# Performance work log

Measured on AMD Instinct MI355X. Metric: run time of the kernel, lower is better.

Reference implementation:

```python
import jax, jax.numpy as jnp
import numpy as np

NUM_HEADS = 16
EMBED = 1024
HEAD = EMBED // NUM_HEADS


def setup_inputs() -> dict:
    key = jax.random.key(0)
    ks = jax.random.split(key, 9)
    s = 1.0 / np.sqrt(EMBED)
    inp = {
        "x": jax.random.normal(ks[0], (2, 2048, EMBED), dtype=jnp.float32),
        "Wq": jax.random.normal(ks[1], (EMBED, EMBED), dtype=jnp.float32) * s,
        "bq": jax.random.normal(ks[2], (EMBED,), dtype=jnp.float32) * s,
        "Wk": jax.random.normal(ks[3], (EMBED, EMBED), dtype=jnp.float32) * s,
        "bk": jax.random.normal(ks[4], (EMBED,), dtype=jnp.float32) * s,
        "Wv": jax.random.normal(ks[5], (EMBED, EMBED), dtype=jnp.float32) * s,
        "bv": jax.random.normal(ks[6], (EMBED,), dtype=jnp.float32) * s,
        "Wo": jax.random.normal(ks[7], (EMBED, EMBED), dtype=jnp.float32) * s,
        "bo": jax.random.normal(ks[8], (EMBED,), dtype=jnp.float32) * s,
    }
    return inp


def reference(x, Wq, bq, Wk, bk, Wv, bv, Wo, bo):
    B, S, E = x.shape
    H, D = NUM_HEADS, HEAD
    # QKV projections ([in,out] layout -> x @ W + b)
    Q = (x @ Wq + bq).reshape(B, S, H, D).transpose(0, 2, 1, 3)  # [B,H,S,D]
    K = (x @ Wk + bk).reshape(B, S, H, D).transpose(0, 2, 1, 3)
    V = (x @ Wv + bv).reshape(B, S, H, D).transpose(0, 2, 1, 3)
    scores = jnp.einsum("bhqd,bhkd->bhqk", Q, K) / jnp.sqrt(jnp.float32(D))
    # causal mask: positions k > q are masked (strict upper triangle)
    causal = jnp.tril(jnp.ones((S, S), dtype=bool))
    scores = jnp.where(causal, scores, jnp.float32(-jnp.inf))
    attn = jax.nn.softmax(scores, axis=-1)
    out = jnp.einsum("bhqk,bhkd->bhqd", attn, V)
    out = out.transpose(0, 2, 1, 3).reshape(B, S, E)
    return out @ Wo + bo
```

## Files before the change

kernel.cpp:

```cpp
#include <hip/hip_runtime.h>


using f32x4  = __attribute__((ext_vector_type(4))) float;
using bf16x8 = __attribute__((ext_vector_type(8))) __bf16;
using u16x8  = __attribute__((ext_vector_type(8))) unsigned short;
using u32x4  = __attribute__((ext_vector_type(4))) unsigned int;

__device__ __forceinline__ unsigned short f2bf(float f) {
  unsigned u = __float_as_uint(f);
  u += 0x7fff + ((u >> 16) & 1u);
  return (unsigned short)(u >> 16);
}

__device__ __forceinline__ unsigned short bfc(float f) {
  __bf16 h = (__bf16)f;
  return __builtin_bit_cast(unsigned short, h);
}

__device__ __forceinline__ bf16x8 ld_bf8(const unsigned short* p) {
  return __builtin_bit_cast(bf16x8, *reinterpret_cast<const u16x8*>(p));
}

#define GLDS16(gp, lp)                                                        \
  __builtin_amdgcn_global_load_lds(                                           \
      (__attribute__((address_space(1))) void*)(gp),                          \
      (__attribute__((address_space(3))) void*)(lp), 16, 0, 0)

__global__ void cast_x_kernel(const float* __restrict__ src,
                              unsigned short* __restrict__ dst) {
  const int i = (blockIdx.x * 256 + threadIdx.x) * 4;
  const float4 v = *reinterpret_cast<const float4*>(src + i);
  ushort4 o;
  o.x = f2bf(v.x); o.y = f2bf(v.y); o.z = f2bf(v.z); o.w = f2bf(v.w);
  *reinterpret_cast<ushort4*>(dst + i) = o;
}

__global__ void cast_wt_kernel(const float* __restrict__ w0, const float* __restrict__ w1,
                               const float* __restrict__ w2, const float* __restrict__ w3,
                               unsigned short* __restrict__ t0, unsigned short* __restrict__ t1,
                               unsigned short* __restrict__ t2, unsigned short* __restrict__ t3) {
  const float* src; unsigned short* dst;
  switch (blockIdx.z) {
    case 0:  src = w0; dst = t0; break;
    case 1:  src = w1; dst = t1; break;
    case 2:  src = w2; dst = t2; break;
    default: src = w3; dst = t3; break;
  }
  __shared__ float tile[64][65];
  const int n0 = blockIdx.x * 64, k0 = blockIdx.y * 64;
  const int t = threadIdx.x;
#pragma unroll
  for (int i = 0; i < 4; ++i) {
    const int q = t + i * 256, r = q >> 4, c4 = q & 15;
    const float4 v = *reinterpret_cast<const float4*>(src + (k0 + r) * 1024 + n0 + c4 * 4);
    tile[r][c4 * 4 + 0] = v.x; tile[r][c4 * 4 + 1] = v.y;
    tile[r][c4 * 4 + 2] = v.z; tile[r][c4 * 4 + 3] = v.w;
  }
  __syncthreads();
#pragma unroll
  for (int i = 0; i < 4; ++i) {
    const int q = t + i * 256, n = q >> 4, c4 = q & 15;
    ushort4 o;
    o.x = f2bf(tile[c4 * 4 + 0][n]); o.y = f2bf(tile[c4 * 4 + 1][n]);
    o.z = f2bf(tile[c4 * 4 + 2][n]); o.w = f2bf(tile[c4 * 4 + 3][n]);
    *reinterpret_cast<ushort4*>(dst + (n0 + n) * 1024 + k0 + c4 * 4) = o;
  }
}

template <int MODE>
__global__ __launch_bounds__(256, 2) void gemm128(
    const unsigned short* __restrict__ A,
    const unsigned short* __restrict__ BtQ, const unsigned short* __restrict__ BtK,
    const unsigned short* __restrict__ BtV,
    const float* __restrict__ biasQ, const float* __restrict__ biasK,
    const float* __restrict__ biasV,
    unsigned short* __restrict__ OQ, unsigned short* __restrict__ OK_,
    unsigned short* __restrict__ OV, float* __restrict__ OF) {
  __shared__ unsigned short As[128 * 64];
  __shared__ unsigned short Bs[128 * 64];

  const int mt = blockIdx.x, nt = blockIdx.y;
  const unsigned short* Bt; const float* bias;
  unsigned short* Obf = nullptr;
  int nloc0;
  float scl = 1.0f;
  if (MODE == 0) {
    const int which = nt >> 3;
    nloc0 = (nt & 7) * 128;
    Bt   = (which == 0) ? BtQ   : (which == 1) ? BtK   : BtV;
    bias = (which == 0) ? biasQ : (which == 1) ? biasK : biasV;
    Obf  = (which == 0) ? OQ    : (which == 1) ? OK_   : OV;
    if (which == 0) scl = 0.18033688f;
  } else {
    nloc0 = nt * 128;
    Bt = BtQ; bias = biasQ;
  }
  const int m0 = mt * 128;
  const int t = threadIdx.x;
  const int w = t >> 6, l = t & 63;
  const int wm = (w >> 1) * 64, wn = (w & 1) * 64;
  const int lr = l & 15, lg = l >> 4;

  f32x4 acc[4][4];
#pragma unroll
  for (int i = 0; i < 4; ++i)
#pragma unroll
    for (int j = 0; j < 4; ++j) acc[i][j] = f32x4{0.f, 0.f, 0.f, 0.f};

  for (int k0 = 0; k0 < 1024; k0 += 64) {
#pragma unroll
    for (int i = 0; i < 4; ++i) {
      const int off = t * 16 + i * 4096;
      const int r = off >> 7, cb = off & 127;
      GLDS16(A + (m0 + r) * 1024 + k0 + (cb >> 1), ((char*)As) + off);
    }
#pragma unroll
    for (int i = 0; i < 4; ++i) {
      const int off = t * 16 + i * 4096;
      const int r = off >> 7, cb = off & 127;
      GLDS16(Bt + (nloc0 + r) * 1024 + k0 + (cb >> 1), ((char*)Bs) + off);
    }
    __syncthreads();
#pragma unroll
    for (int kk = 0; kk < 2; ++kk) {
      bf16x8 af[4], bfr[4];
#pragma unroll
      for (int mi = 0; mi < 4; ++mi)
        af[mi] = ld_bf8(As + (wm + mi * 16 + lr) * 64 + kk * 32 + lg * 8);
#pragma unroll
      for (int ni = 0; ni < 4; ++ni)
        bfr[ni] = ld_bf8(Bs + (wn + ni * 16 + lr) * 64 + kk * 32 + lg * 8);
#pragma unroll
      for (int mi = 0; mi < 4; ++mi)
#pragma unroll
        for (int ni = 0; ni < 4; ++ni)
          acc[mi][ni] = __builtin_amdgcn_mfma_f32_16x16x32_bf16(af[mi], bfr[ni], acc[mi][ni], 0, 0, 0);
    }
    __syncthreads();
  }

#pragma unroll
  for (int ni = 0; ni < 4; ++ni) {
    const int n = nloc0 + wn + ni * 16 + lr;
    const float bv = bias[n];
#pragma unroll
    for (int mi = 0; mi < 4; ++mi) {
#pragma unroll
      for (int r = 0; r < 4; ++r) {
        const int m = m0 + wm + mi * 16 + 4 * lg + r;
        const float v = (acc[mi][ni][r] + bv) * scl;
        if (MODE == 0) {
          const int b = m >> 11, s = m & 2047;
          const int h = n >> 6,  d = n & 63;
          Obf[(((b * 16 + h) * 2048) + s) * 64 + d] = f2bf(v);
        } else {
          OF[m * 1024 + n] = v;
        }
      }
    }
  }
}

__global__ void transpose_v_kernel(const unsigned short* __restrict__ Vh,
                                   unsigned short* __restrict__ Vt) {
  const int bh = blockIdx.y;
  const int s0 = blockIdx.x * 64;
  __shared__ unsigned short tile[64][72];
  const int t = threadIdx.x;
#pragma unroll
  for (int i = 0; i < 4; ++i) {
    const int q = t + i * 256, r = q >> 4, c4 = q & 15;
    const ushort4 v = *reinterpret_cast<const ushort4*>(Vh + ((size_t)bh * 2048 + s0 + r) * 64 + c4 * 4);
    tile[r][c4 * 4 + 0] = v.x; tile[r][c4 * 4 + 1] = v.y;
    tile[r][c4 * 4 + 2] = v.z; tile[r][c4 * 4 + 3] = v.w;
  }
  __syncthreads();
#pragma unroll
  for (int i = 0; i < 4; ++i) {
    const int q = t + i * 256, d = q >> 4, c4 = q & 15;
    ushort4 o;
    o.x = tile[c4 * 4 + 0][d]; o.y = tile[c4 * 4 + 1][d];
    o.z = tile[c4 * 4 + 2][d]; o.w = tile[c4 * 4 + 3][d];
    *reinterpret_cast<ushort4*>(Vt + ((size_t)bh * 64 + d) * 2048 + s0 + c4 * 4) = o;
  }
}

__global__ __launch_bounds__(256, 4) void attn_kernel(
    const unsigned short* __restrict__ Qh, const unsigned short* __restrict__ Kh,
    const unsigned short* __restrict__ Vt, unsigned short* __restrict__ Ob) {
  const int g = blockIdx.x;
  const int qt = 31 - (g >> 5);
  const int bh = g & 31;
  const int b = bh >> 4, h = bh & 15;
  const int t = threadIdx.x, w = t >> 6, l = t & 63;
  const int lr = l & 15, lg = l >> 4;
  const int sl0 = lr + 32 * (lg & 1);
  const int sl1 = sl0 + 16;
  const bool hi2 = (l & 32) != 0;

  __shared__ unsigned short Kb[2][4096];
  __shared__ unsigned short Vb[2][4096];

  const unsigned short* Kbase = Kh + (size_t)bh * (2048 * 64);
  const unsigned short* Vbase = Vt + (size_t)bh * (64 * 2048);

  const int qb = qt * 64 + w * 16;
  const unsigned short* Qp = Qh + ((size_t)bh * 2048 + qb + lr) * 64;
  bf16x8 qf[2];
  qf[0] = ld_bf8(Qp + lg * 8);
  qf[1] = ld_bf8(Qp + 32 + lg * 8);

  f32x4 oacc[4];
#pragma unroll
  for (int i = 0; i < 4; ++i) oacc[i] = f32x4{0.f, 0.f, 0.f, 0.f};
  float mrun = -3e38f;
  float lpart = 0.f;

  auto stage = [&](int kv0, int bi) {
#pragma unroll
    for (int p = 0; p < 2; ++p) {
      const int o = t * 16 + p * 4096;
      const int row = o >> 7;
      const int scb = (o & 127) ^ ((row & 7) << 4);
      GLDS16(Kbase + (size_t)(kv0 + row) * 64 + (scb >> 1), ((char*)Kb[bi]) + o);
      GLDS16(Vbase + (size_t)row * 2048 + kv0 + (scb >> 1), ((char*)Vb[bi]) + o);
    }
  };

  const int nt = qt + 1;
  stage(0, 0);
  __syncthreads();

  for (int ti = 0; ti < nt; ++ti) {
    const int cur = ti & 1;
    const int kv0 = ti * 64;
    if (ti + 1 < nt) stage((ti + 1) * 64, cur ^ 1);

    f32x4 s[4];
#pragma unroll
    for (int i = 0; i < 4; ++i) s[i] = f32x4{0.f, 0.f, 0.f, 0.f};
    __builtin_amdgcn_s_setprio(1);
#pragma unroll
    for (int kf = 0; kf < 2; ++kf) {
#pragma unroll
      for (int nf = 0; nf < 4; ++nf) {
        const int row = nf * 16 + lr;
        const int col = (kf * 32 + lg * 8) ^ ((row & 7) << 3);
        const bf16x8 kb = ld_bf8(&Kb[cur][row * 64 + col]);
        s[nf] = __builtin_amdgcn_mfma_f32_16x16x32_bf16(kb, qf[kf], s[nf], 0, 0, 0);
      }
    }
    __builtin_amdgcn_s_setprio(0);

    if (ti == qt) {
#pragma unroll
      for (int nf = 0; nf < 4; ++nf) {
        const int kv = kv0 + nf * 16 + 4 * lg;
#pragma unroll
        for (int r = 0; r < 4; ++r)
          if (kv + r > qb + lr) s[nf][r] = -3e38f;
      }
    }
    float m01 = -3e38f, m23 = -3e38f;
#pragma unroll
    for (int r = 0; r < 4; ++r) {
      m01 = fmaxf(m01, fmaxf(s[0][r], s[1][r]));
      m23 = fmaxf(m23, fmaxf(s[2][r], s[3][r]));
    }
    const float mx = fmaxf(m01, m23);
    if (!__all(mx <= mrun + 8.f)) {
      float m0 = fmaxf(mx, __shfl_xor(mx, 16));
      m0 = fmaxf(m0, __shfl_xor(m0, 32));
      const float n0 = fmaxf(mrun, m0);
      const float c0 = __builtin_amdgcn_exp2f(mrun - n0);
      mrun = n0;
      lpart *= c0;
#pragma unroll
      for (int df = 0; df < 4; ++df)
#pragma unroll
        for (int r = 0; r < 4; ++r) oacc[df][r] *= c0;
    }
    float rs[4] = {0.f, 0.f, 0.f, 0.f};
#pragma unroll
    for (int nf = 0; nf < 4; ++nf)
#pragma unroll
      for (int r = 0; r < 4; ++r) {
        const float p = __builtin_amdgcn_exp2f(s[nf][r] - mrun);
        s[nf][r] = p;
        rs[nf] += p;
      }
    lpart += (rs[0] + rs[1]) + (rs[2] + rs[3]);

    unsigned wpk[4][2];
#pragma unroll
    for (int nf = 0; nf < 4; ++nf) {
      asm("v_cvt_pk_bf16_f32 %0, %1, %2" : "=v"(wpk[nf][0]) : "v"(s[nf][0]), "v"(s[nf][1]));
      asm("v_cvt_pk_bf16_f32 %0, %1, %2" : "=v"(wpk[nf][1]) : "v"(s[nf][2]), "v"(s[nf][3]));
    }
    bf16x8 pa[2];
#pragma unroll
    for (int kf = 0; kf < 2; ++kf) {
      const unsigned a0w = __shfl(wpk[2 * kf][0], sl0), b0w = __shfl(wpk[2 * kf + 1][0], sl0);
      const unsigned a1w = __shfl(wpk[2 * kf][1], sl0), b1w = __shfl(wpk[2 * kf + 1][1], sl0);
      const unsigned a2w = __shfl(wpk[2 * kf][0], sl1), b2w = __shfl(wpk[2 * kf + 1][0], sl1);
      const unsigned a3w = __shfl(wpk[2 * kf][1], sl1), b3w = __shfl(wpk[2 * kf + 1][1], sl1);
      u32x4 uu;
      uu[0] = hi2 ? b0w : a0w;
      uu[1] = hi2 ? b1w : a1w;
      uu[2] = hi2 ? b2w : a2w;
      uu[3] = hi2 ? b3w : a3w;
      pa[kf] = __builtin_bit_cast(bf16x8, uu);
    }

    __builtin_amdgcn_s_setprio(1);
#pragma unroll
    for (int kf = 0; kf < 2; ++kf) {
#pragma unroll
      for (int df = 0; df < 4; ++df) {
        const int vrow = df * 16 + lr;
        const int vcol = (kf * 32 + lg * 8) ^ ((vrow & 7) << 3);
        const bf16x8 vb = ld_bf8(&Vb[cur][vrow * 64 + vcol]);
        oacc[df] = __builtin_amdgcn_mfma_f32_16x16x32_bf16(vb, pa[kf], oacc[df], 0, 0, 0);
      }
    }
    __builtin_amdgcn_s_setprio(0);
    __syncthreads();
  }

  float ls = lpart;
  ls += __shfl_xor(ls, 16);
  ls += __shfl_xor(ls, 32);
  const float inv = 1.f / ls;
  const int q = qb + lr;
#pragma unroll
  for (int df = 0; df < 4; ++df) {
    ushort4 o4;
    o4.x = bfc(oacc[df][0] * inv);
    o4.y = bfc(oacc[df][1] * inv);
    o4.z = bfc(oacc[df][2] * inv);
    o4.w = bfc(oacc[df][3] * inv);
    *reinterpret_cast<ushort4*>(
        &Ob[((size_t)(b * 2048 + q)) * 1024 + h * 64 + df * 16 + 4 * lg]) = o4;
  }
}

extern "C" void kernel_launch(void* const* d_in, const int* in_sizes, int n_in,
                              void* d_out, int out_size, void* d_ws, size_t ws_size,
                              hipStream_t stream) {
  const float* x  = (const float*)d_in[0];
  const float* Wq = (const float*)d_in[1];
  const float* bq = (const float*)d_in[2];
  const float* Wk = (const float*)d_in[3];
  const float* bk = (const float*)d_in[4];
  const float* Wv = (const float*)d_in[5];
  const float* bv = (const float*)d_in[6];
  const float* Wo = (const float*)d_in[7];
  const float* bo = (const float*)d_in[8];
  float* out = (float*)d_out;

  unsigned short* xb  = (unsigned short*)d_ws;
  unsigned short* wqt = xb  + 4096 * 1024;
  unsigned short* wkt = wqt + 1024 * 1024;
  unsigned short* wvt = wkt + 1024 * 1024;
  unsigned short* wot = wvt + 1024 * 1024;
  unsigned short* Qh  = wot + 1024 * 1024;
  unsigned short* Kh  = Qh  + 4096 * 1024;
  unsigned short* Vh  = Kh  + 4096 * 1024;
  unsigned short* Vt  = Vh  + 4096 * 1024;
  unsigned short* Ob  = Vt  + 4096 * 1024;

  cast_x_kernel<<<4096, 256, 0, stream>>>(x, xb);
  cast_wt_kernel<<<dim3(16, 16, 4), 256, 0, stream>>>(Wq, Wk, Wv, Wo, wqt, wkt, wvt, wot);
  gemm128<0><<<dim3(32, 24), 256, 0, stream>>>(xb, wqt, wkt, wvt, bq, bk, bv,
                                               Qh, Kh, Vh, nullptr);
  transpose_v_kernel<<<dim3(32, 32), 256, 0, stream>>>(Vh, Vt);
  attn_kernel<<<1024, 256, 0, stream>>>(Qh, Kh, Vt, Ob);
  gemm128<1><<<dim3(32, 8), 256, 0, stream>>>(Ob, wot, nullptr, nullptr, bo, nullptr, nullptr,
                                              nullptr, nullptr, nullptr, out);
}
```

Before: 121.2 us.

## Merge cast kernels, write V transposed from QKV GEMM, use 256-tile pipelined GEMM

Combines the x cast and weight transpose-casts into one launch. Replaces the 128x128 QKV GEMM with a 256x256 tile, 512-thread kernel that uses a 4-stage global-to-LDS pipeline, XOR-swizzled LDS, setprio around the MFMA blocks and a block-index remap. The V projection is now written straight into the transposed layout, so the separate transpose kernel and its extra pass over V are gone. The output projection becomes its own specialized kernel with occupancy raised to 3. The larger tiles cut global traffic and launch count, but the QKV GEMM now runs only 192 blocks at 1 block per CU, which may leave CUs underused.

```diff
diff --git a/kernel.cpp b/kernel.cpp
--- a/kernel.cpp
+++ b/kernel.cpp
@@ -26,29 +26,33 @@
       (__attribute__((address_space(1))) void*)(gp),                          \
       (__attribute__((address_space(3))) void*)(lp), 16, 0, 0)
 
-__global__ void cast_x_kernel(const float* __restrict__ src,
-                              unsigned short* __restrict__ dst) {
-  const int i = (blockIdx.x * 256 + threadIdx.x) * 4;
-  const float4 v = *reinterpret_cast<const float4*>(src + i);
-  ushort4 o;
-  o.x = f2bf(v.x); o.y = f2bf(v.y); o.z = f2bf(v.z); o.w = f2bf(v.w);
-  *reinterpret_cast<ushort4*>(dst + i) = o;
-}
-
-__global__ void cast_wt_kernel(const float* __restrict__ w0, const float* __restrict__ w1,
-                               const float* __restrict__ w2, const float* __restrict__ w3,
-                               unsigned short* __restrict__ t0, unsigned short* __restrict__ t1,
-                               unsigned short* __restrict__ t2, unsigned short* __restrict__ t3) {
+__global__ void prep_kernel(const float* __restrict__ x,
+                            const float* __restrict__ w0, const float* __restrict__ w1,
+                            const float* __restrict__ w2, const float* __restrict__ w3,
+                            unsigned short* __restrict__ xb,
+                            unsigned short* __restrict__ t0, unsigned short* __restrict__ t1,
+                            unsigned short* __restrict__ t2, unsigned short* __restrict__ t3) {
+  __shared__ float tile[64][65];
+  const int t = threadIdx.x;
+  const int bid = blockIdx.x;
+  if (bid < 4096) {
+    const int i = (bid * 256 + t) * 4;
+    const float4 v = *reinterpret_cast<const float4*>(x + i);
+    ushort4 o;
+    o.x = f2bf(v.x); o.y = f2bf(v.y); o.z = f2bf(v.z); o.w = f2bf(v.w);
+    *reinterpret_cast<ushort4*>(xb + i) = o;
+    return;
+  }
+  const int q0 = bid - 4096;
+  const int wsel = q0 >> 8, rem = q0 & 255;
   const float* src; unsigned short* dst;
-  switch (blockIdx.z) {
+  switch (wsel) {
     case 0:  src = w0; dst = t0; break;
     case 1:  src = w1; dst = t1; break;
     case 2:  src = w2; dst = t2; break;
     default: src = w3; dst = t3; break;
   }
-  __shared__ float tile[64][65];
-  const int n0 = blockIdx.x * 64, k0 = blockIdx.y * 64;
-  const int t = threadIdx.x;
+  const int n0 = (rem & 15) * 64, k0 = (rem >> 4) * 64;
 #pragma unroll
   for (int i = 0; i < 4; ++i) {
     const int q = t + i * 256, r = q >> 4, c4 = q & 15;
@@ -67,35 +71,152 @@
   }
 }
 
-template <int MODE>
-__global__ __launch_bounds__(256, 2) void gemm128(
+__global__ __launch_bounds__(512, 1) void gemm256_qkv(
     const unsigned short* __restrict__ A,
     const unsigned short* __restrict__ BtQ, const unsigned short* __restrict__ BtK,
     const unsigned short* __restrict__ BtV,
     const float* __restrict__ biasQ, const float* __restrict__ biasK,
     const float* __restrict__ biasV,
     unsigned short* __restrict__ OQ, unsigned short* __restrict__ OK_,
-    unsigned short* __restrict__ OV, float* __restrict__ OF) {
+    unsigned short* __restrict__ OVt) {
+  __shared__ unsigned short As[4][256 * 32];
+  __shared__ unsigned short Bs[4][256 * 32];
+
+  const int bid0 = blockIdx.x;
+  const int bid = (bid0 & 7) * 24 + (bid0 >> 3);
+  const int ntile = bid >> 4;
+  const int mtile = bid & 15;
+  const int which = ntile >> 2;
+  const unsigned short* Bt = (which == 0) ? BtQ : (which == 1) ? BtK : BtV;
+  const float* bias = (which == 0) ? biasQ : (which == 1) ? biasK : biasV;
+  const int nn = (ntile & 3) * 256;
+  const int m0 = mtile * 256;
+
+  const int tid = threadIdx.x;
+  const int w = tid >> 6, l = tid & 63;
+  const int wm = (w >> 2) * 128, wn = (w & 3) * 64;
+  const int lr = l & 15, lg = l >> 4;
+
+  f32x4 acc[8][4];
+#pragma unroll
+  for (int i = 0; i < 8; ++i)
+#pragma unroll
+    for (int j = 0; j < 4; ++j) acc[i][j] = f32x4{0.f, 0.f, 0.f, 0.f};
+
+  auto stA = [&](int kt) {
+    const int s = kt & 3;
+#pragma unroll
+    for (int p = 0; p < 2; ++p) {
+      const int o = tid * 16 + p * 8192;
+      const int row = o >> 6, cb = o & 63;
+      const int scb = cb ^ (((row >> 1) & 3) << 4);
+      GLDS16(A + (size_t)(m0 + row) * 1024 + kt * 32 + (scb >> 1),
+             ((char*)As[s]) + o);
+    }
+  };
+  auto stB = [&](int kt) {
+    const int s = kt & 3;
+#pragma unroll
+    for (int p = 0; p < 2; ++p) {
+      const int o = tid * 16 + p * 8192;
+      const int row = o >> 6, cb = o & 63;
+      const int scb = cb ^ (((row >> 1) & 3) << 4);
+      GLDS16(Bt + (size_t)(nn + row) * 1024 + kt * 32 + (scb >> 1),
+             ((char*)Bs[s]) + o);
+    }
+  };
+
+  stA(0); stB(0); stA(1); stB(1); stA(2); stB(2);
+  asm volatile("s_waitcnt vmcnt(8)" ::: "memory");
+  __builtin_amdgcn_s_barrier();
+
+  for (int kt = 0; kt < 32; ++kt) {
+    const int s = kt & 3;
+    const unsigned short* as = As[s];
+    const unsigned short* bs = Bs[s];
+    bf16x8 bfr[4], af[4];
+#pragma unroll
+    for (int nf = 0; nf < 4; ++nf) {
+      const int row = wn + nf * 16 + lr;
+      bfr[nf] = ld_bf8(bs + row * 32 + (lg * 8 ^ (((row >> 1) & 3) << 3)));
+    }
+#pragma unroll
+    for (int mi = 0; mi < 4; ++mi) {
+      const int row = wm + mi * 16 + lr;
+      af[mi] = ld_bf8(as + row * 32 + (lg * 8 ^ (((row >> 1) & 3) << 3)));
+    }
+    if (kt + 3 < 32) stA(kt + 3);
+    asm volatile("" ::: "memory");
+    __builtin_amdgcn_s_barrier();
+    asm volatile("s_waitcnt lgkmcnt(0)" ::: "memory");
+    __builtin_amdgcn_sched_barrier(0);
+    __builtin_amdgcn_s_setprio(1);
+#pragma unroll
+    for (int mi = 0; mi < 4; ++mi)
+#pragma unroll
+      for (int nf = 0; nf < 4; ++nf)
+        acc[mi][nf] = __builtin_amdgcn_mfma_f32_16x16x32_bf16(af[mi], bfr[nf], acc[mi][nf], 0, 0, 0);
+    __builtin_amdgcn_s_setprio(0);
+    __builtin_amdgcn_s_barrier();
+#pragma unroll
+    for (int mi = 0; mi < 4; ++mi) {
+      const int row = wm + 64 + mi * 16 + lr;
+      af[mi] = ld_bf8(as + row * 32 + (lg * 8 ^ (((row >> 1) & 3) << 3)));
+    }
+    if (kt + 3 < 32) stB(kt + 3);
+    asm volatile("" ::: "memory");
+    __builtin_amdgcn_s_barrier();
+    asm volatile("s_waitcnt lgkmcnt(0)" ::: "memory");
+    __builtin_amdgcn_sched_barrier(0);
+    __builtin_amdgcn_s_setprio(1);
+#pragma unroll
+    for (int mi = 0; mi < 4; ++mi)
+#pragma unroll
+      for (int nf = 0; nf < 4; ++nf)
+        acc[4 + mi][nf] = __builtin_amdgcn_mfma_f32_16x16x32_bf16(af[mi], bfr[nf], acc[4 + mi][nf], 0, 0, 0);
+    __builtin_amdgcn_s_setprio(0);
+    asm volatile("s_waitcnt vmcnt(8)" ::: "memory");
+    __builtin_amdgcn_s_barrier();
+  }
+
+  const float SC = (which == 0) ? 0.18033688f : 1.0f;
+  unsigned short* Oqk = (which == 0) ? OQ : OK_;
+#pragma unroll
+  for (int nf = 0; nf < 4; ++nf) {
+    const int n = nn + wn + nf * 16 + lr;
+    const float bv = bias[n];
+    const int hh = n >> 6, dd = n & 63;
+#pragma unroll
+    for (int mi = 0; mi < 8; ++mi) {
+      const int mB = m0 + wm + mi * 16 + 4 * lg;
+      const int bb = mB >> 11, sloc = mB & 2047;
+      if (which == 2) {
+        ushort4 o4;
+        o4.x = bfc(acc[mi][nf][0] + bv);
+        o4.y = bfc(acc[mi][nf][1] + bv);
+        o4.z = bfc(acc[mi][nf][2] + bv);
+        o4.w = bfc(acc[mi][nf][3] + bv);
+        *reinterpret_cast<ushort4*>(
+            &OVt[(((size_t)(bb * 16 + hh)) * 64 + dd) * 2048 + sloc]) = o4;
+      } else {
+#pragma unroll
+        for (int r = 0; r < 4; ++r) {
+          const float v = (acc[mi][nf][r] + bv) * SC;
+          Oqk[(((size_t)(bb * 16 + hh)) * 2048 + sloc + r) * 64 + dd] = f2bf(v);
+        }
+      }
+    }
+  }
+}
+
+__global__ __launch_bounds__(256, 3) void gemm_out(
+    const unsigned short* __restrict__ A, const unsigned short* __restrict__ Bt,
+    const float* __restrict__ bias, float* __restrict__ OF) {
   __shared__ unsigned short As[128 * 64];
   __shared__ unsigned short Bs[128 * 64];
 
-  const int mt = blockIdx.x, nt = blockIdx.y;
-  const unsigned short* Bt; const float* bias;
-  unsigned short* Obf = nullptr;
-  int nloc0;
-  float scl = 1.0f;
-  if (MODE == 0) {
-    const int which = nt >> 3;
-    nloc0 = (nt & 7) * 128;
-    Bt   = (which == 0) ? BtQ   : (which == 1) ? BtK   : BtV;
-    bias = (which == 0) ? biasQ : (which == 1) ? biasK : biasV;
-    Obf  = (which == 0) ? OQ    : (which == 1) ? OK_   : OV;
-    if (which == 0) scl = 0.18033688f;
-  } else {
-    nloc0 = nt * 128;
-    Bt = BtQ; bias = biasQ;
-  }
-  const int m0 = mt * 128;
+  const int m0 = blockIdx.x * 128;
+  const int nloc0 = blockIdx.y * 128;
   const int t = threadIdx.x;
   const int w = t >> 6, l = t & 63;
   const int wm = (w >> 1) * 64, wn = (w & 1) * 64;
@@ -148,40 +269,9 @@
 #pragma unroll
       for (int r = 0; r < 4; ++r) {
         const int m = m0 + wm + mi * 16 + 4 * lg + r;
-        const float v = (acc[mi][ni][r] + bv) * scl;
-        if (MODE == 0) {
-          const int b = m >> 11, s = m & 2047;
-          const int h = n >> 6,  d = n & 63;
-          Obf[(((b * 16 + h) * 2048) + s) * 64 + d] = f2bf(v);
-        } else {
-          OF[m * 1024 + n] = v;
-        }
-      }
-    }
-  }
-}
-
-__global__ void transpose_v_kernel(const unsigned short* __restrict__ Vh,
-                                   unsigned short* __restrict__ Vt) {
-  const int bh = blockIdx.y;
-  const int s0 = blockIdx.x * 64;
-  __shared__ unsigned short tile[64][72];
-  const int t = threadIdx.x;
-#pragma unroll
-  for (int i = 0; i < 4; ++i) {
-    const int q = t + i * 256, r = q >> 4, c4 = q & 15;
-    const ushort4 v = *reinterpret_cast<const ushort4*>(Vh + ((size_t)bh * 2048 + s0 + r) * 64 + c4 * 4);
-    tile[r][c4 * 4 + 0] = v.x; tile[r][c4 * 4 + 1] = v.y;
-    tile[r][c4 * 4 + 2] = v.z; tile[r][c4 * 4 + 3] = v.w;
-  }
-  __syncthreads();
-#pragma unroll
-  for (int i = 0; i < 4; ++i) {
-    const int q = t + i * 256, d = q >> 4, c4 = q & 15;
-    ushort4 o;
-    o.x = tile[c4 * 4 + 0][d]; o.y = tile[c4 * 4 + 1][d];
-    o.z = tile[c4 * 4 + 2][d]; o.w = tile[c4 * 4 + 3][d];
-    *reinterpret_cast<ushort4*>(Vt + ((size_t)bh * 64 + d) * 2048 + s0 + c4 * 4) = o;
+        OF[m * 1024 + n] = acc[mi][ni][r] + bv;
+      }
+    }
   }
 }
 
@@ -369,12 +459,8 @@
   unsigned short* Vt  = Vh  + 4096 * 1024;
   unsigned short* Ob  = Vt  + 4096 * 1024;
 
-  cast_x_kernel<<<4096, 256, 0, stream>>>(x, xb);
-  cast_wt_kernel<<<dim3(16, 16, 4), 256, 0, stream>>>(Wq, Wk, Wv, Wo, wqt, wkt, wvt, wot);
-  gemm128<0><<<dim3(32, 24), 256, 0, stream>>>(xb, wqt, wkt, wvt, bq, bk, bv,
-                                               Qh, Kh, Vh, nullptr);
-  transpose_v_kernel<<<dim3(32, 32), 256, 0, stream>>>(Vh, Vt);
+  prep_kernel<<<5120, 256, 0, stream>>>(x, Wq, Wk, Wv, Wo, xb, wqt, wkt, wvt, wot);
+  gemm256_qkv<<<192, 512, 0, stream>>>(xb, wqt, wkt, wvt, bq, bk, bv, Qh, Kh, Vt);
   attn_kernel<<<1024, 256, 0, stream>>>(Qh, Kh, Vt, Ob);
-  gemm128<1><<<dim3(32, 8), 256, 0, stream>>>(Ob, wot, nullptr, nullptr, bo, nullptr, nullptr,
-                                              nullptr, nullptr, nullptr, out);
-}
+  gemm_out<<<dim3(32, 8), 256, 0, stream>>>(Ob, wot, bo, out);
+}
```

Result: no change. 120.8 us (-0.4%).

## Fuse prep casts, write V transposed from GEMM, software-pipeline PV MFMA

Applied to the files above, without the earlier changes.

Merges the x cast and weight transpose-cast kernels into one launch. The QKV GEMM epilogue now writes V directly in transposed [bh,d,s] layout, which removes the separate transpose kernel and its extra round trip through memory. In attention, the PV MFMAs of the previous tile are deferred and issued alongside the next tile's QK MFMAs, with V fragments preloaded into registers so matrix work overlaps the softmax. This raises register pressure in the attention kernel and makes the V epilogue stores strided.

```diff
diff --git a/kernel.cpp b/kernel.cpp
--- a/kernel.cpp
+++ b/kernel.cpp
@@ -26,29 +26,33 @@
       (__attribute__((address_space(1))) void*)(gp),                          \
       (__attribute__((address_space(3))) void*)(lp), 16, 0, 0)
 
-__global__ void cast_x_kernel(const float* __restrict__ src,
-                              unsigned short* __restrict__ dst) {
-  const int i = (blockIdx.x * 256 + threadIdx.x) * 4;
-  const float4 v = *reinterpret_cast<const float4*>(src + i);
-  ushort4 o;
-  o.x = f2bf(v.x); o.y = f2bf(v.y); o.z = f2bf(v.z); o.w = f2bf(v.w);
-  *reinterpret_cast<ushort4*>(dst + i) = o;
-}
-
-__global__ void cast_wt_kernel(const float* __restrict__ w0, const float* __restrict__ w1,
-                               const float* __restrict__ w2, const float* __restrict__ w3,
-                               unsigned short* __restrict__ t0, unsigned short* __restrict__ t1,
-                               unsigned short* __restrict__ t2, unsigned short* __restrict__ t3) {
+__global__ void prep_kernel(const float* __restrict__ x,
+                            const float* __restrict__ w0, const float* __restrict__ w1,
+                            const float* __restrict__ w2, const float* __restrict__ w3,
+                            unsigned short* __restrict__ xb,
+                            unsigned short* __restrict__ t0, unsigned short* __restrict__ t1,
+                            unsigned short* __restrict__ t2, unsigned short* __restrict__ t3) {
+  __shared__ float tile[64][65];
+  const int t = threadIdx.x;
+  const int bid = blockIdx.x;
+  if (bid < 4096) {
+    const int i = (bid * 256 + t) * 4;
+    const float4 v = *reinterpret_cast<const float4*>(x + i);
+    ushort4 o;
+    o.x = f2bf(v.x); o.y = f2bf(v.y); o.z = f2bf(v.z); o.w = f2bf(v.w);
+    *reinterpret_cast<ushort4*>(xb + i) = o;
+    return;
+  }
+  const int q0 = bid - 4096;
+  const int wsel = q0 >> 8, rem = q0 & 255;
   const float* src; unsigned short* dst;
-  switch (blockIdx.z) {
+  switch (wsel) {
     case 0:  src = w0; dst = t0; break;
     case 1:  src = w1; dst = t1; break;
     case 2:  src = w2; dst = t2; break;
     default: src = w3; dst = t3; break;
   }
-  __shared__ float tile[64][65];
-  const int n0 = blockIdx.x * 64, k0 = blockIdx.y * 64;
-  const int t = threadIdx.x;
+  const int n0 = (rem & 15) * 64, k0 = (rem >> 4) * 64;
 #pragma unroll
   for (int i = 0; i < 4; ++i) {
     const int q = t + i * 256, r = q >> 4, c4 = q & 15;
@@ -75,22 +79,18 @@
     const float* __restrict__ biasQ, const float* __restrict__ biasK,
     const float* __restrict__ biasV,
     unsigned short* __restrict__ OQ, unsigned short* __restrict__ OK_,
-    unsigned short* __restrict__ OV, float* __restrict__ OF) {
+    unsigned short* __restrict__ OVt, float* __restrict__ OF) {
   __shared__ unsigned short As[128 * 64];
   __shared__ unsigned short Bs[128 * 64];
 
   const int mt = blockIdx.x, nt = blockIdx.y;
   const unsigned short* Bt; const float* bias;
-  unsigned short* Obf = nullptr;
-  int nloc0;
-  float scl = 1.0f;
+  int nloc0, which = 0;
   if (MODE == 0) {
-    const int which = nt >> 3;
+    which = nt >> 3;
     nloc0 = (nt & 7) * 128;
     Bt   = (which == 0) ? BtQ   : (which == 1) ? BtK   : BtV;
     bias = (which == 0) ? biasQ : (which == 1) ? biasK : biasV;
-    Obf  = (which == 0) ? OQ    : (which == 1) ? OK_   : OV;
-    if (which == 0) scl = 0.18033688f;
   } else {
     nloc0 = nt * 128;
     Bt = BtQ; bias = biasQ;
@@ -139,49 +139,40 @@
     __syncthreads();
   }
 
+  const float scl = (MODE == 0 && which == 0) ? 0.18033688f : 1.0f;
 #pragma unroll
   for (int ni = 0; ni < 4; ++ni) {
     const int n = nloc0 + wn + ni * 16 + lr;
     const float bv = bias[n];
 #pragma unroll
     for (int mi = 0; mi < 4; ++mi) {
-#pragma unroll
-      for (int r = 0; r < 4; ++r) {
-        const int m = m0 + wm + mi * 16 + 4 * lg + r;
-        const float v = (acc[mi][ni][r] + bv) * scl;
-        if (MODE == 0) {
-          const int b = m >> 11, s = m & 2047;
-          const int h = n >> 6,  d = n & 63;
-          Obf[(((b * 16 + h) * 2048) + s) * 64 + d] = f2bf(v);
-        } else {
-          OF[m * 1024 + n] = v;
+      const int mB = m0 + wm + mi * 16 + 4 * lg;
+      if (MODE == 0 && which == 2) {
+        const int bb = mB >> 11, sloc = mB & 2047;
+        const int hh = n >> 6, dd = n & 63;
+        ushort4 o4;
+        o4.x = bfc(acc[mi][ni][0] + bv);
+        o4.y = bfc(acc[mi][ni][1] + bv);
+        o4.z = bfc(acc[mi][ni][2] + bv);
+        o4.w = bfc(acc[mi][ni][3] + bv);
+        *reinterpret_cast<ushort4*>(
+            &OVt[(((size_t)(bb * 16 + hh)) * 64 + dd) * 2048 + sloc]) = o4;
+      } else {
+#pragma unroll
+        for (int r = 0; r < 4; ++r) {
+          const int m = mB + r;
+          const float v = (acc[mi][ni][r] + bv) * scl;
+          if (MODE == 0) {
+            const int bb = m >> 11, sloc = m & 2047;
+            const int hh = n >> 6, dd = n & 63;
+            unsigned short* Oqk = (which == 0) ? OQ : OK_;
+            Oqk[(((size_t)(bb * 16 + hh)) * 2048 + sloc) * 64 + dd] = f2bf(v);
+          } else {
+            OF[m * 1024 + n] = v;
+          }
         }
       }
     }
-  }
-}
-
-__global__ void transpose_v_kernel(const unsigned short* __restrict__ Vh,
-                                   unsigned short* __restrict__ Vt) {
-  const int bh = blockIdx.y;
-  const int s0 = blockIdx.x * 64;
-  __shared__ unsigned short tile[64][72];
-  const int t = threadIdx.x;
-#pragma unroll
-  for (int i = 0; i < 4; ++i) {
-    const int q = t + i * 256, r = q >> 4, c4 = q & 15;
-    const ushort4 v = *reinterpret_cast<const ushort4*>(Vh + ((size_t)bh * 2048 + s0 + r) * 64 + c4 * 4);
-    tile[r][c4 * 4 + 0] = v.x; tile[r][c4 * 4 + 1] = v.y;
-    tile[r][c4 * 4 + 2] = v.z; tile[r][c4 * 4 + 3] = v.w;
-  }
-  __syncthreads();
-#pragma unroll
-  for (int i = 0; i < 4; ++i) {
-    const int q = t + i * 256, d = q >> 4, c4 = q & 15;
-    ushort4 o;
-    o.x = tile[c4 * 4 + 0][d]; o.y = tile[c4 * 4 + 1][d];
-    o.z = tile[c4 * 4 + 2][d]; o.w = tile[c4 * 4 + 3][d];
-    *reinterpret_cast<ushort4*>(Vt + ((size_t)bh * 64 + d) * 2048 + s0 + c4 * 4) = o;
   }
 }
 
@@ -216,6 +207,9 @@
   float mrun = -3e38f;
   float lpart = 0.f;
 
+  bf16x8 vbp[2][4];
+  bf16x8 pap[2];
+
   auto stage = [&](int kv0, int bi) {
 #pragma unroll
     for (int p = 0; p < 2; ++p) {
@@ -250,7 +244,23 @@
         s[nf] = __builtin_amdgcn_mfma_f32_16x16x32_bf16(kb, qf[kf], s[nf], 0, 0, 0);
       }
     }
+    if (ti > 0) {
+#pragma unroll
+      for (int kf = 0; kf < 2; ++kf)
+#pragma unroll
+        for (int df = 0; df < 4; ++df)
+          oacc[df] = __builtin_amdgcn_mfma_f32_16x16x32_bf16(vbp[kf][df], pap[kf], oacc[df], 0, 0, 0);
+    }
     __builtin_amdgcn_s_setprio(0);
+
+#pragma unroll
+    for (int kf = 0; kf < 2; ++kf)
+#pragma unroll
+      for (int df = 0; df < 4; ++df) {
+        const int vrow = df * 16 + lr;
+        const int vcol = (kf * 32 + lg * 8) ^ ((vrow & 7) << 3);
+        vbp[kf][df] = ld_bf8(&Vb[cur][vrow * 64 + vcol]);
+      }
 
     if (ti == qt) {
 #pragma unroll
@@ -297,7 +307,6 @@
       asm("v_cvt_pk_bf16_f32 %0, %1, %2" : "=v"(wpk[nf][0]) : "v"(s[nf][0]), "v"(s[nf][1]));
       asm("v_cvt_pk_bf16_f32 %0, %1, %2" : "=v"(wpk[nf][1]) : "v"(s[nf][2]), "v"(s[nf][3]));
     }
-    bf16x8 pa[2];
 #pragma unroll
     for (int kf = 0; kf < 2; ++kf) {
       const unsigned a0w = __shfl(wpk[2 * kf][0], sl0), b0w = __shfl(wpk[2 * kf + 1][0], sl0);
@@ -309,23 +318,16 @@
       uu[1] = hi2 ? b1w : a1w;
       uu[2] = hi2 ? b2w : a2w;
       uu[3] = hi2 ? b3w : a3w;
-      pa[kf] = __builtin_bit_cast(bf16x8, uu);
-    }
-
-    __builtin_amdgcn_s_setprio(1);
-#pragma unroll
-    for (int kf = 0; kf < 2; ++kf) {
-#pragma unroll
-      for (int df = 0; df < 4; ++df) {
-        const int vrow = df * 16 + lr;
-        const int vcol = (kf * 32 + lg * 8) ^ ((vrow & 7) << 3);
-        const bf16x8 vb = ld_bf8(&Vb[cur][vrow * 64 + vcol]);
-        oacc[df] = __builtin_amdgcn_mfma_f32_16x16x32_bf16(vb, pa[kf], oacc[df], 0, 0, 0);
-      }
-    }
-    __builtin_amdgcn_s_setprio(0);
+      pap[kf] = __builtin_bit_cast(bf16x8, uu);
+    }
     __syncthreads();
   }
+
+#pragma unroll
+  for (int kf = 0; kf < 2; ++kf)
+#pragma unroll
+    for (int df = 0; df < 4; ++df)
+      oacc[df] = __builtin_amdgcn_mfma_f32_16x16x32_bf16(vbp[kf][df], pap[kf], oacc[df], 0, 0, 0);
 
   float ls = lpart;
   ls += __shfl_xor(ls, 16);
@@ -369,11 +371,9 @@
   unsigned short* Vt  = Vh  + 4096 * 1024;
   unsigned short* Ob  = Vt  + 4096 * 1024;
 
-  cast_x_kernel<<<4096, 256, 0, stream>>>(x, xb);
-  cast_wt_kernel<<<dim3(16, 16, 4), 256, 0, stream>>>(Wq, Wk, Wv, Wo, wqt, wkt, wvt, wot);
+  prep_kernel<<<5120, 256, 0, stream>>>(x, Wq, Wk, Wv, Wo, xb, wqt, wkt, wvt, wot);
   gemm128<0><<<dim3(32, 24), 256, 0, stream>>>(xb, wqt, wkt, wvt, bq, bk, bv,
-                                               Qh, Kh, Vh, nullptr);
-  transpose_v_kernel<<<dim3(32, 32), 256, 0, stream>>>(Vh, Vt);
+                                               Qh, Kh, Vt, nullptr);
   attn_kernel<<<1024, 256, 0, stream>>>(Qh, Kh, Vt, Ob);
   gemm128<1><<<dim3(32, 8), 256, 0, stream>>>(Ob, wot, nullptr, nullptr, bo, nullptr, nullptr,
                                               nullptr, nullptr, nullptr, out);
```

Measured after the change: 113.3 us. 6.5% less time.
